# Performance work log

Hardware: AMD Instinct MI355X
Metric: run time of the kernel (lower is better)

The kernel has to match this reference:

```python
import jax, jax.numpy as jnp
from jax import lax
import numpy as np

V, T, K, R, H, EN, L = 10000, 100, 50, 300, 200, 800, 3
B = 128
TRAIN_SIZE = 100000
DELTA = 0.005


def setup_inputs():
    key = jax.random.key(0)
    ks = jax.random.split(key, 16)
    s = 0.02
    return {
        "bows": jax.random.uniform(ks[0], (B, V), jnp.float32) * 10.0 + 1e-3,
        "times": jax.random.randint(ks[1], (B,), 0, T),
        "rnn_inp": jax.random.uniform(ks[2], (T, V), jnp.float32),
        "rho_W": jax.random.normal(ks[3], (V, R), jnp.float32) * s,
        "mu_q_alpha": jax.random.normal(ks[4], (K, T, R), jnp.float32),
        "logsigma_q_alpha": jax.random.normal(ks[5], (K, T, R), jnp.float32) * 0.1 - 2.0,
        "qtheta_W1": jax.random.normal(ks[6], (EN, V + K), jnp.float32) * s,
        "qtheta_b1": jnp.zeros((EN,), jnp.float32),
        "qtheta_W2": jax.random.normal(ks[7], (EN, EN), jnp.float32) * s,
        "qtheta_b2": jnp.zeros((EN,), jnp.float32),
        "mu_theta_W": jax.random.normal(ks[8], (K, EN), jnp.float32) * s,
        "mu_theta_b": jnp.zeros((K,), jnp.float32),
        "ls_theta_W": jax.random.normal(ks[9], (K, EN), jnp.float32) * s,
        "ls_theta_b": jnp.zeros((K,), jnp.float32),
        "eta_map_W": jax.random.normal(ks[10], (H, V), jnp.float32) * s,
        "eta_map_b": jnp.zeros((H,), jnp.float32),
        "lstm_Wih": jax.random.normal(ks[11], (L, 4 * H, H), jnp.float32) * s,
        "lstm_Whh": jax.random.normal(ks[12], (L, 4 * H, H), jnp.float32) * s,
        "lstm_bih": jnp.zeros((L, 4 * H), jnp.float32),
        "lstm_bhh": jnp.zeros((L, 4 * H), jnp.float32),
        "mu_eta_W": jax.random.normal(ks[13], (K, H + K), jnp.float32) * s,
        "mu_eta_b": jnp.zeros((K,), jnp.float32),
        "ls_eta_W": jax.random.normal(ks[14], (K, H + K), jnp.float32) * s,
        "ls_eta_b": jnp.zeros((K,), jnp.float32),
    }


def _kl(q_mu, q_ls, p_mu, p_ls):
    # KL(N(q_mu, exp(q_ls)) || N(p_mu, exp(p_ls))), logsigma == log-variance as in torch code
    return 0.5 * jnp.sum((jnp.exp(q_ls) + (q_mu - p_mu) ** 2) / (jnp.exp(p_ls) + 1e-6) - 1.0 + p_ls - q_ls, axis=-1)


def _lstm(x, Wih, Whh, bih, bhh):
    # x: [T, H]; L stacked LSTM layers (batch of 1 squeezed), torch gate order i,f,g,o
    for l in range(Wih.shape[0]):
        Wi, Wh, bi, bh = Wih[l], Whh[l], bih[l], bhh[l]
        Hd = Wh.shape[1]

        def step(carry, xt, Wi=Wi, Wh=Wh, bi=bi, bh=bh):
            h, c = carry
            g = Wi @ xt + Wh @ h + bi + bh
            i, f, gg, o = jnp.split(g, 4)
            c = jax.nn.sigmoid(f) * c + jax.nn.sigmoid(i) * jnp.tanh(gg)
            h = jax.nn.sigmoid(o) * jnp.tanh(c)
            return (h, c), h

        z = jnp.zeros((Hd,), x.dtype)
        _, x = lax.scan(step, (z, z), x)
    return x


def _forward(bows, rnn_inp, rho_W, mu_q_alpha, logsigma_q_alpha, qtheta_W1, qtheta_b1, qtheta_W2, qtheta_b2, mu_theta_W, mu_theta_b, ls_theta_W, ls_theta_b, eta_map_W, eta_map_b, lstm_Wih, lstm_Whh, lstm_bih, lstm_bhh, mu_eta_W, mu_eta_b, ls_eta_W, ls_eta_b, times):
    log_delta = jnp.log(jnp.float32(DELTA))
    # --- eta: LSTM over word-freq sequence, then sequential mu/logsigma/KL per t ---
    out = _lstm(rnn_inp @ eta_map_W.T + eta_map_b, lstm_Wih, lstm_Whh, lstm_bih, lstm_bhh)  # [T,H]
    p_ls_seq = jnp.concatenate([jnp.zeros((1,), jnp.float32), jnp.full((T - 1,), log_delta, jnp.float32)])

    def eta_step(eta_prev, xs):
        o_t, p_ls = xs
        x = jnp.concatenate([o_t, eta_prev])
        mu = mu_eta_W @ x + mu_eta_b
        ls = ls_eta_W @ x + ls_eta_b
        kl = _kl(mu, ls, eta_prev, jnp.full_like(mu, p_ls))
        return mu, (mu, kl)  # eval-mode reparameterize -> eta_t = mu

    _, (etas, kls) = lax.scan(eta_step, jnp.zeros((K,), jnp.float32), (out, p_ls_seq))
    kl_eta = kls.sum()
    # --- theta encoder ---
    nb = bows / bows.sum(1, keepdims=True)
    eta_td = etas[times]  # [B,K]
    h = jax.nn.relu(jnp.concatenate([nb, eta_td], axis=1) @ qtheta_W1.T + qtheta_b1)
    h = jax.nn.relu(h @ qtheta_W2.T + qtheta_b2)
    mu_t = h @ mu_theta_W.T + mu_theta_b
    ls_t = h @ ls_theta_W.T + ls_theta_b
    theta = jax.nn.softmax(mu_t, axis=-1)  # z = mu (eval-mode reparam)
    coeff = jnp.float32(TRAIN_SIZE / bows.shape[0])
    kl_theta = _kl(mu_t, ls_t, eta_td, jnp.zeros_like(mu_t)).sum() * coeff
    # --- alpha: with eval-mode reparam, alphas == mu, so KL is fully vectorized ---
    muT = jnp.transpose(mu_q_alpha, (1, 0, 2))  # [T,K,R]
    lsT = jnp.transpose(logsigma_q_alpha, (1, 0, 2))
    alphas = muT
    p_mu = jnp.concatenate([jnp.zeros((1, K, R), muT.dtype), alphas[:-1]], axis=0)
    p_ls = jnp.concatenate([jnp.zeros((1, K, R), muT.dtype), jnp.full((T - 1, K, R), log_delta, muT.dtype)], axis=0)
    kl_alpha = _kl(muT, lsT, p_mu, p_ls).sum()
    # --- beta and NLL ---
    logit = alphas.reshape(T * K, R) @ rho_W.T  # [T*K, V]
    beta = jax.nn.softmax(logit, axis=-1).reshape(T, K, V)
    beta_d = beta[times]  # [B,K,V]
    loglik = jnp.log(jnp.einsum('bk,bkv->bv', theta, beta_d) + 1e-12)
    nll = (-(loglik * bows).sum(-1)).sum() * coeff
    loss = nll + kl_eta + kl_theta + kl_alpha
    return loss, nll, kl_eta, kl_theta, kl_alpha


def reference(bows, times, rnn_inp, rho_W, mu_q_alpha, logsigma_q_alpha, qtheta_W1, qtheta_b1, qtheta_W2, qtheta_b2, mu_theta_W, mu_theta_b, ls_theta_W, ls_theta_b, eta_map_W, eta_map_b, lstm_Wih, lstm_Whh, lstm_bih, lstm_bhh, mu_eta_W, mu_eta_b, ls_eta_W, ls_eta_b):
    return _forward(bows, rnn_inp, rho_W, mu_q_alpha, logsigma_q_alpha, qtheta_W1, qtheta_b1, qtheta_W2, qtheta_b2, mu_theta_W, mu_theta_b, ls_theta_W, ls_theta_b, eta_map_W, eta_map_b, lstm_Wih, lstm_Whh, lstm_bih, lstm_bhh, mu_eta_W, mu_eta_b, ls_eta_W, ls_eta_b, times)
```

## Files before the change

### kernel.cpp

```cpp
#include <hip/hip_runtime.h>


typedef unsigned int u32;
typedef unsigned short u16;
typedef _Float16 f16;
typedef f16 f16x2 __attribute__((ext_vector_type(2)));
typedef short bf16x8 __attribute__((ext_vector_type(8)));
typedef float f32x4 __attribute__((ext_vector_type(4)));
typedef u32 u32x4 __attribute__((ext_vector_type(4)));

#define LOG_DELTA (-5.2983174f)
#define COEFF 781.25f

#if defined(__has_builtin)
#if __has_builtin(__builtin_amdgcn_sdot4)
#define HAVE_SDOT4 1
#endif
#endif

__device__ __forceinline__ float bf2f(u16 a) { return __uint_as_float(((u32)a) << 16); }
__device__ __forceinline__ u16 f2bf(float f) {
  u32 u = __float_as_uint(f);
  u32 r = (u + 0x7fffu + ((u >> 16) & 1u)) >> 16;
  return (u16)r;
}
__device__ __forceinline__ int dot4i8(u32 a, u32 b, int c) {
#ifdef HAVE_SDOT4
  return __builtin_amdgcn_sdot4(a, b, c, false);
#else
  int s = c;
  s += ((int)(a << 24) >> 24) * ((int)(b << 24) >> 24);
  s += ((int)(a << 16) >> 24) * ((int)(b << 16) >> 24);
  s += ((int)(a << 8) >> 24) * ((int)(b << 8) >> 24);
  s += ((int)a >> 24) * ((int)b >> 24);
  return s;
#endif
}
__device__ __forceinline__ float sigm(float x) { return 1.f / (1.f + __expf(-x)); }
__device__ __forceinline__ float ftanh(float x) { float t = __expf(2.f * x); return (t - 1.f) / (t + 1.f); }
__device__ __forceinline__ u16 f2h(float x) { return __builtin_bit_cast(u16, (f16)x); }
__device__ __forceinline__ float h2f(u16 x) { return (float)__builtin_bit_cast(f16, x); }
__device__ __forceinline__ void async_load16(const u16* g, u16* l) {
  __builtin_amdgcn_global_load_lds((const __attribute__((address_space(1))) u32*)g,
                                   (__attribute__((address_space(3))) u32*)l, 16, 0, 0);
}


__global__ __launch_bounds__(64) void k_zero(float* __restrict__ accum) {
  if (threadIdx.x < 8) accum[threadIdx.x] = 0.f;
}

__global__ __launch_bounds__(256) void k_nb(const float* __restrict__ bows, float* __restrict__ nb) {
  __shared__ float red[256];
  const int b = blockIdx.x, tid = threadIdx.x;
  float s = 0.f;
  for (int v = tid; v < 10000; v += 256) s += bows[b * 10000 + v];
  red[tid] = s; __syncthreads();
  for (int o = 128; o > 0; o >>= 1) { if (tid < o) red[tid] += red[tid + o]; __syncthreads(); }
  const float inv = 1.f / red[0];
  for (int v = tid; v < 10000; v += 256) nb[b * 10000 + v] = bows[b * 10000 + v] * inv;
}

__global__ __launch_bounds__(256) void k_bsum(const float* __restrict__ a, const float* __restrict__ b,
                                              float* __restrict__ o, int n) {
  int i = blockIdx.x * 256 + threadIdx.x;
  if (i < n) o[i] = a[i] + b[i];
}

__global__ __launch_bounds__(256) void k_fill(float* __restrict__ C, const float* __restrict__ bias,
                                              int N, int total) {
  for (int i = blockIdx.x * 256 + threadIdx.x; i < total; i += gridDim.x * 256)
    C[i] = bias[i % N];
}

__global__ __launch_bounds__(256) void k_relu(float* __restrict__ C, int total) {
  for (int i = blockIdx.x * 256 + threadIdx.x; i < total; i += gridDim.x * 256) {
    float v = C[i];
    C[i] = v > 0.f ? v : 0.f;
  }
}

__global__ __launch_bounds__(128) void k_stack2(const float* __restrict__ a, const float* __restrict__ b,
                                                float* __restrict__ o) {
  const int t = threadIdx.x;
  if (t < 50) o[t] = a[t];
  else if (t < 100) o[t] = b[t - 50];
}

__global__ __launch_bounds__(64) void k_quant_whh(const float* __restrict__ Whh,
                                                  u32* __restrict__ whq, float* __restrict__ rowscale) {
  const int gr = blockIdx.x;
  const int lane = threadIdx.x;
  __shared__ float wrow[200];
  const float* src = Whh + (size_t)gr * 200;
  float m = 0.f;
  for (int c = lane; c < 200; c += 64) { float v = src[c]; wrow[c] = v; m = fmaxf(m, fabsf(v)); }
  for (int o = 32; o > 0; o >>= 1) m = fmaxf(m, __shfl_down(m, o));
  m = __shfl(m, 0);
  const float qs = (m > 0.f) ? 127.f / m : 0.f;
  __syncthreads();
  const int l = gr / 800, rr = gr - l * 800;
  if (lane < 52) {
    u32 d = 0;
    if (lane < 50) {
#pragma unroll
      for (int b = 0; b < 4; ++b) {
        int q = __float2int_rn(wrow[lane * 4 + b] * qs);
        q = max(-127, min(127, q));
        d |= ((u32)(q & 0xff)) << (8 * b);
      }
    }
    whq[l * 41600 + rr * 52 + lane] = d;
  }
  if (lane == 0) rowscale[gr] = (m > 0.f) ? m / 127.f : 0.f;
}

__global__ __launch_bounds__(256) void k_prep_A(const float* __restrict__ muq, u16* __restrict__ Abf) {
  int idx = blockIdx.x * 256 + threadIdx.x;
  if (idx >= 5120 * 320) return;
  int r = idx % 320, m = idx / 320;
  float v = 0.f;
  if (r < 300 && m < 5000) { int t = m / 50, k = m - t * 50; v = muq[k * 30000 + t * 300 + r]; }
  Abf[idx] = f2bf(v);
}
__global__ __launch_bounds__(256) void k_prep_B(const float* __restrict__ rho, u16* __restrict__ Bbf) {
  int idx = blockIdx.x * 256 + threadIdx.x;
  if (idx >= 10112 * 320) return;
  int r = idx % 320, n = idx / 320;
  float v = (r < 300 && n < 10000) ? rho[n * 300 + r] : 0.f;
  Bbf[idx] = f2bf(v);
}


#define ST 64
#define SBK 32

template<int AMODE, int BMODE, int EPI>
__global__ __launch_bounds__(256) void gemm64(
    const float* __restrict__ A, const float* __restrict__ Bm, const float* __restrict__ Bm2,
    const float* __restrict__ bias, float* __restrict__ C,
    int M, int N, int Kd, int lda, int ldb,
    const int* __restrict__ times, const float* __restrict__ etas)
{
  __shared__ __align__(16) float As[SBK][ST + 4];
  __shared__ __align__(16) float Bs[SBK][ST + 4];
  const int tid = threadIdx.x;
  const int tx = tid & 15, ty = tid >> 4;
  const int m_base = blockIdx.x * ST, n_base = blockIdx.y * ST;
  float acc[4][4] = {};
  const int nkt = (Kd + SBK - 1) / SBK;
  const int per = (nkt + gridDim.z - 1) / gridDim.z;
  const int kt0 = blockIdx.z * per;
  const int kt1 = min(nkt, kt0 + per);
  const int lkk = tid & 31;
  const int lrow = tid >> 5;
  for (int kt = kt0; kt < kt1; ++kt) {
    const int kg = kt * SBK + lkk;
#pragma unroll
    for (int i = 0; i < 8; ++i) {
      const int m = m_base + lrow + i * 8;
      float v = 0.f;
      if (m < M && kg < Kd) {
        if (AMODE == 0) v = A[(size_t)m * lda + kg];
        else {
          if (kg < 10000) v = A[(size_t)m * 10000 + kg];
          else v = etas[times[m] * 50 + (kg - 10000)];
        }
      }
      As[lkk][lrow + i * 8] = v;
    }
#pragma unroll
    for (int i = 0; i < 8; ++i) {
      const int n = n_base + lrow + i * 8;
      float v = 0.f;
      if (n < N && kg < Kd) {
        if (BMODE == 0) v = Bm[(size_t)n * ldb + kg];
        else v = (n < 50) ? Bm[(size_t)n * ldb + kg] : Bm2[(size_t)(n - 50) * ldb + kg];
      }
      Bs[lkk][lrow + i * 8] = v;
    }
    __syncthreads();
#pragma unroll
    for (int kk = 0; kk < SBK; ++kk) {
      const float4 a4 = *(const float4*)&As[kk][ty * 4];
      const float4 b4 = *(const float4*)&Bs[kk][tx * 4];
      const float av[4] = {a4.x, a4.y, a4.z, a4.w};
      const float bv[4] = {b4.x, b4.y, b4.z, b4.w};
#pragma unroll
      for (int i = 0; i < 4; ++i)
#pragma unroll
        for (int j = 0; j < 4; ++j) acc[i][j] += av[i] * bv[j];
    }
    __syncthreads();
  }
#pragma unroll
  for (int i = 0; i < 4; ++i) {
    const int m = m_base + ty * 4 + i;
    if (m >= M) continue;
#pragma unroll
    for (int j = 0; j < 4; ++j) {
      const int n = n_base + tx * 4 + j;
      if (n >= N) continue;
      float v = acc[i][j];
      if (EPI == 1) { C[(size_t)m * N + n] = v + bias[n]; }
      else if (EPI == 2) { v += bias[n]; C[(size_t)m * N + n] = v > 0.f ? v : 0.f; }
      else if (EPI == 5) { atomicAdd(&C[(size_t)m * N + n], v); }
      else { C[(size_t)m * N + n] = v; }
    }
  }
}


__global__ __launch_bounds__(256) void gemm_mfma_bT(
    const u16* __restrict__ A, const u16* __restrict__ B, u16* __restrict__ C,
    int M, int N)
{
  __shared__ u16 As[128 * 32];
  __shared__ u16 Bs[128 * 32];
  const int tid = threadIdx.x;
  const int l = tid & 63, w = tid >> 6;
  const int wm = w & 1, wn = w >> 1;
  const int m0 = blockIdx.x * 128, n0 = blockIdx.y * 128;
  f32x4 acc[4][4] = {};
  const int arow = l >> 2;
  const int acol = (l & 3) * 8;
  for (int kt = 0; kt < 10; ++kt) {
    const int k0 = kt * 32;
#pragma unroll
    for (int c = 0; c < 2; ++c) {
      const int i = w + c * 4;
      async_load16(A + (size_t)(m0 + i * 16 + arow) * 320 + k0 + acol, As + i * 512);
      async_load16(B + (size_t)(n0 + i * 16 + arow) * 320 + k0 + acol, Bs + i * 512);
    }
    __syncthreads();
    bf16x8 af[4], bfr[4];
#pragma unroll
    for (int x = 0; x < 4; ++x) {
      af[x]  = *(const bf16x8*)&As[(wm * 64 + x * 16 + (l & 15)) * 32 + (l >> 4) * 8];
      bfr[x] = *(const bf16x8*)&Bs[(wn * 64 + x * 16 + (l & 15)) * 32 + (l >> 4) * 8];
    }
#pragma unroll
    for (int x = 0; x < 4; ++x)
#pragma unroll
      for (int y = 0; y < 4; ++y)
        acc[x][y] = __builtin_amdgcn_mfma_f32_16x16x32_bf16(af[x], bfr[y], acc[x][y], 0, 0, 0);
    __syncthreads();
  }
  const int col = l & 15, quad = l >> 4;
#pragma unroll
  for (int x = 0; x < 4; ++x) {
    const int gmB = m0 + wm * 64 + x * 16 + quad * 4;
#pragma unroll
    for (int y = 0; y < 4; ++y) {
      const int gn = n0 + wn * 64 + y * 16 + col;
      if (gn >= N) continue;
#pragma unroll
      for (int r = 0; r < 4; ++r) {
        const int gm = gmB + r;
        if (gm < M) C[(size_t)gm * N + gn] = f2bf(acc[x][y][r]);
      }
    }
  }
}


__global__ __launch_bounds__(512, 1) void lstm_scan_reg(
    const u32* __restrict__ whq,
    const float* __restrict__ rowscale,
    const float* __restrict__ xproj,
    float* __restrict__ hseq)
{
  __shared__ u16 pg[800];
  __shared__ __align__(16) u32 hq[52];
  __shared__ float wmax[8];
  __shared__ float hscale_s[1];
  const int tid = threadIdx.x;
  const int act = (tid < 400);
  const int r0 = tid, r1 = tid + 400;
  u32x4 wA4[13], wB4[13];
  float rsA = 0.f, rsB = 0.f;
  float xpA = 0.f, xpB = 0.f;
  if (act) {
    const u32x4* gA = (const u32x4*)(whq + (size_t)r0 * 52);
    const u32x4* gB = (const u32x4*)(whq + (size_t)r1 * 52);
#pragma unroll
    for (int i = 0; i < 13; ++i) { wA4[i] = gA[i]; wB4[i] = gB[i]; }
    rsA = rowscale[r0]; rsB = rowscale[r1];
    xpA = xproj[r0]; xpB = xproj[r1];
  }
  if (tid < 52) hq[tid] = 0;
  if (tid < 8) wmax[tid] = 0.f;
  if (tid == 0) hscale_s[0] = 0.f;
  float c_reg = 0.f;
  __syncthreads();
  for (int t = 0; t < 100; ++t) {
    if (act) {
      float nxA = 0.f, nxB = 0.f;
      if (t < 99) { nxA = xproj[(t + 1) * 800 + r0]; nxB = xproj[(t + 1) * 800 + r1]; }
      const float hdq = hscale_s[0];
      u32x4 hv4[13];
#pragma unroll
      for (int i = 0; i < 13; ++i) hv4[i] = *((const u32x4*)hq + i);
      int aA = 0, aB = 0;
#pragma unroll
      for (int g = 0; g < 50; ++g) {
        const u32 h = hv4[g >> 2][g & 3];
        aA = dot4i8(wA4[g >> 2][g & 3], h, aA);
        aB = dot4i8(wB4[g >> 2][g & 3], h, aB);
      }
      pg[r0] = f2h((float)aA * (rsA * hdq) + xpA);
      pg[r1] = f2h((float)aB * (rsB * hdq) + xpB);
      xpA = nxA; xpB = nxB;
    }
    __syncthreads();
    float hv = 0.f;
    if (tid < 200) {
      float gi = sigm(h2f(pg[tid]));
      float gf = sigm(h2f(pg[200 + tid]));
      float gg = ftanh(h2f(pg[400 + tid]));
      float go = sigm(h2f(pg[600 + tid]));
      c_reg = gf * c_reg + gi * gg;
      hv = go * ftanh(c_reg);
      hseq[t * 200 + tid] = hv;
    }
    float m = fabsf(hv);
    for (int o = 32; o > 0; o >>= 1) m = fmaxf(m, __shfl_down(m, o));
    if ((tid & 63) == 0) wmax[tid >> 6] = m;
    __syncthreads();
    if (tid < 200) {
      const float hm = fmaxf(fmaxf(wmax[0], wmax[1]), fmaxf(wmax[2], wmax[3]));
      const float qs = (hm > 0.f) ? 127.f / hm : 0.f;
      int q = __float2int_rn(hv * qs);
      q = max(-127, min(127, q));
      ((signed char*)hq)[tid] = (signed char)q;
      if (tid == 0) hscale_s[0] = (hm > 0.f) ? hm / 127.f : 0.f;
    }
    __syncthreads();
  }
}


__global__ __launch_bounds__(64, 1) void eta_scan_reg(
    const float* __restrict__ muW, const float* __restrict__ lsW,
    const float* __restrict__ pc0,
    float* __restrict__ etas, float* __restrict__ accum)
{
  __shared__ __align__(16) float ep[52];
  const int j = threadIdx.x;
  const int act = (j < 50);
  float wmu[52], wls[52];
  if (act) {
#pragma unroll
    for (int k = 0; k < 25; ++k) {
      float2 a = *(const float2*)(muW + (size_t)j * 250 + 200 + 2 * k);
      float2 b = *(const float2*)(lsW + (size_t)j * 250 + 200 + 2 * k);
      wmu[2 * k] = a.x; wmu[2 * k + 1] = a.y;
      wls[2 * k] = b.x; wls[2 * k + 1] = b.y;
    }
    wmu[50] = wmu[51] = wls[50] = wls[51] = 0.f;
  } else {
#pragma unroll
    for (int k = 0; k < 52; ++k) { wmu[k] = 0.f; wls[k] = 0.f; }
  }
  if (j < 52) ep[j] = 0.f;
  float klacc = 0.f;
  float mye = 0.f;
  float pmu = act ? pc0[j] : 0.f;
  float pls_ = act ? pc0[50 + j] : 0.f;
  __syncthreads();
  for (int t = 0; t < 100; ++t) {
    float nmu = 0.f, nls = 0.f;
    if (act && t < 99) { nmu = pc0[(t + 1) * 100 + j]; nls = pc0[(t + 1) * 100 + 50 + j]; }
    float ma[4] = {pmu, 0.f, 0.f, 0.f};
    float la[4] = {pls_, 0.f, 0.f, 0.f};
    const float4* e4 = (const float4*)ep;
#pragma unroll
    for (int i = 0; i < 13; ++i) {
      const float4 e = e4[i];
      ma[0] += wmu[4 * i + 0] * e.x; ma[1] += wmu[4 * i + 1] * e.y;
      ma[2] += wmu[4 * i + 2] * e.z; ma[3] += wmu[4 * i + 3] * e.w;
      la[0] += wls[4 * i + 0] * e.x; la[1] += wls[4 * i + 1] * e.y;
      la[2] += wls[4 * i + 2] * e.z; la[3] += wls[4 * i + 3] * e.w;
    }
    const float mu = (ma[0] + ma[1]) + (ma[2] + ma[3]);
    const float ls = (la[0] + la[1]) + (la[2] + la[3]);
    __syncthreads();
    if (act) {
      const float pls = (t == 0) ? 0.f : LOG_DELTA;
      const float pv = __expf(pls) + 1e-6f;
      const float d = mu - mye;
      klacc += 0.5f * ((__expf(ls) + d * d) / pv - 1.f + pls - ls);
      etas[t * 50 + j] = mu;
      mye = mu;
      ep[j] = mu;
    }
    __syncthreads();
    pmu = nmu; pls_ = nls;
  }
  for (int o = 32; o > 0; o >>= 1) klacc += __shfl_down(klacc, o);
  if (j == 0) accum[0] = klacc;
}


__global__ __launch_bounds__(64) void k_theta(const float* __restrict__ mul,
                                              const float* __restrict__ etas, const int* __restrict__ times,
                                              float* __restrict__ theta, float* __restrict__ accum) {
  const int b = blockIdx.x, lane = threadIdx.x;
  float m_ = 0.f, l_ = 0.f, e_ = 0.f, mx = -1e30f;
  if (lane < 50) {
    m_ = mul[b * 100 + lane];
    l_ = mul[b * 100 + 50 + lane];
    e_ = etas[times[b] * 50 + lane];
    mx = m_;
  }
  for (int o = 32; o > 0; o >>= 1) mx = fmaxf(mx, __shfl_down(mx, o));
  mx = __shfl(mx, 0);
  float ex = (lane < 50) ? __expf(m_ - mx) : 0.f;
  float sum = ex;
  for (int o = 32; o > 0; o >>= 1) sum += __shfl_down(sum, o);
  sum = __shfl(sum, 0);
  if (lane < 50) theta[b * 50 + lane] = ex / sum;
  float kl = 0.f;
  if (lane < 50) {
    float d = m_ - e_;
    kl = 0.5f * ((__expf(l_) + d * d) / (1.f + 1e-6f) - 1.f - l_);
  }
  for (int o = 32; o > 0; o >>= 1) kl += __shfl_down(kl, o);
  if (lane == 0) atomicAdd(accum + 1, kl);
}


__global__ __launch_bounds__(256) void k_rowsum(const u16* __restrict__ logit, float* __restrict__ Z) {
  const int r = blockIdx.x, tid = threadIdx.x;
  const u32* row = (const u32*)(logit + (size_t)r * 10000);
  __shared__ float red[256];
  float s = 0.f;
  for (int v = tid; v < 5000; v += 256) {
    u32 p = row[v];
    s += __expf(bf2f((u16)(p & 0xffffu))) + __expf(bf2f((u16)(p >> 16)));
  }
  red[tid] = s; __syncthreads();
  for (int o = 128; o > 0; o >>= 1) { if (tid < o) red[tid] += red[tid + o]; __syncthreads(); }
  if (tid == 0) Z[r] = red[0];
}


__global__ __launch_bounds__(256) void k_nll(const u16* __restrict__ logit, const float* __restrict__ Z,
                                             const float* __restrict__ theta, const float* __restrict__ bows,
                                             const int* __restrict__ times, float* __restrict__ accum) {
  const int b = blockIdx.x, seg = blockIdx.y, tid = threadIdx.x;
  const int t = times[b];
  __shared__ float c2[52];
  __shared__ float red[256];
  if (tid < 50) c2[tid] = theta[b * 50 + tid] / Z[t * 50 + tid];
  __syncthreads();
  float part = 0.f;
  const int v0 = seg * 1250, v1 = v0 + 1250;
  const u16* base = logit + (size_t)t * 500000;
  for (int v = v0 + tid; v < v1; v += 256) {
    float ssv = 1e-12f;
#pragma unroll
    for (int k = 0; k < 50; ++k) ssv += c2[k] * __expf(bf2f(base[k * 10000 + v]));
    part += bows[b * 10000 + v] * __logf(ssv);
  }
  red[tid] = part; __syncthreads();
  for (int o = 128; o > 0; o >>= 1) { if (tid < o) red[tid] += red[tid + o]; __syncthreads(); }
  if (tid == 0) atomicAdd(accum + 3, -red[0]);
}


__global__ __launch_bounds__(256) void k_alpha_kl(const float* __restrict__ muq, const float* __restrict__ lsq,
                                                  float* __restrict__ accum) {
  __shared__ float red[256];
  const int tid = threadIdx.x;
  float s = 0.f;
  for (int i = blockIdx.x * 256 + tid; i < 1500000; i += gridDim.x * 256) {
    int r = i % 300;
    int tk = i / 300;
    int k = tk % 50;
    int t = tk / 50;
    size_t idx = (size_t)k * 30000 + (size_t)t * 300 + r;
    float mu = muq[idx], ls = lsq[idx];
    float pm = 0.f, pls = 0.f;
    if (t > 0) { pm = muq[idx - 300]; pls = LOG_DELTA; }
    float d = mu - pm;
    s += 0.5f * ((__expf(ls) + d * d) / (__expf(pls) + 1e-6f) - 1.f + pls - ls);
  }
  red[tid] = s; __syncthreads();
  for (int o = 128; o > 0; o >>= 1) { if (tid < o) red[tid] += red[tid + o]; __syncthreads(); }
  if (tid == 0) atomicAdd(accum + 2, red[0]);
}


__global__ __launch_bounds__(64) void k_final(const float* __restrict__ accum, float* __restrict__ out) {
  if (threadIdx.x == 0) {
    float nll = accum[3] * COEFF;
    float kl_eta = accum[0];
    float kl_theta = accum[1] * COEFF;
    float kl_alpha = accum[2];
    out[0] = nll + kl_eta + kl_theta + kl_alpha;
    out[1] = nll;
    out[2] = kl_eta;
    out[3] = kl_theta;
    out[4] = kl_alpha;
  }
}


extern "C" void kernel_launch(void* const* d_in, const int* in_sizes, int n_in,
                              void* d_out, int out_size, void* d_ws, size_t ws_size,
                              hipStream_t stream) {
  (void)in_sizes; (void)n_in; (void)out_size; (void)ws_size;
  const float* bows   = (const float*)d_in[0];
  const int*   times  = (const int*)d_in[1];
  const float* rnn_in = (const float*)d_in[2];
  const float* rho_W  = (const float*)d_in[3];
  const float* muq    = (const float*)d_in[4];
  const float* lsq    = (const float*)d_in[5];
  const float* qW1    = (const float*)d_in[6];
  const float* qb1    = (const float*)d_in[7];
  const float* qW2    = (const float*)d_in[8];
  const float* qb2    = (const float*)d_in[9];
  const float* muthW  = (const float*)d_in[10];
  const float* muthb  = (const float*)d_in[11];
  const float* lsthW  = (const float*)d_in[12];
  const float* lsthb  = (const float*)d_in[13];
  const float* emW    = (const float*)d_in[14];
  const float* emb    = (const float*)d_in[15];
  const float* Wih    = (const float*)d_in[16];
  const float* Whh    = (const float*)d_in[17];
  const float* bih    = (const float*)d_in[18];
  const float* bhh    = (const float*)d_in[19];
  const float* mueW   = (const float*)d_in[20];
  const float* mueb   = (const float*)d_in[21];
  const float* lseW   = (const float*)d_in[22];
  const float* lseb   = (const float*)d_in[23];
  float* out = (float*)d_out;
  float* ws = (float*)d_ws;

  float* accum = ws + 0;
  float* nb    = ws + 8;
  float* x0    = ws + 1280008;
  float* xproj = ws + 1300008;
  float* hsA   = ws + 1380008;
  float* hsB   = ws + 1400008;
  u32*   whq   = (u32*)(ws + 1420008);
  float* rowsc = ws + 1544808;
  float* bias2 = ws + 1547208;
  float* pc0   = ws + 1547408;
  float* bias2e= ws + 1558008;
  float* hsC   = ws + 1560008;
  float* bsum  = ws + 1660008;
  float* etas  = ws + 1662408;
  float* h1    = ws + 1667408;
  float* h2    = ws + 1769808;
  float* mul   = ws + 1872208;
  float* theta = ws + 1885008;
  float* Zrow  = ws + 1891408;
  u16*   A_bf  = (u16*)(ws + 1896408);
  u16*   B_bf  = (u16*)(ws + 2715608);
  u16*   logit = (u16*)(ws + 4333528);

  k_zero<<<1, 64, 0, stream>>>(accum);
  k_nb<<<128, 256, 0, stream>>>(bows, nb);
  k_quant_whh<<<2400, 64, 0, stream>>>(Whh, whq, rowsc);
  k_bsum<<<10, 256, 0, stream>>>(bih, bhh, bsum, 2400);
  k_prep_A<<<6400, 256, 0, stream>>>(muq, A_bf);
  k_prep_B<<<12640, 256, 0, stream>>>(rho_W, B_bf);
  k_stack2<<<1, 128, 0, stream>>>(muthb, lsthb, bias2);
  k_stack2<<<1, 128, 0, stream>>>(mueb, lseb, bias2e);
  k_fill<<<40, 256, 0, stream>>>(pc0, bias2e, 100, 10000);

  k_fill<<<79, 256, 0, stream>>>(x0, emb, 200, 20000);
  gemm64<0, 0, 5><<<dim3(2, 4, 32), 256, 0, stream>>>(rnn_in, emW, nullptr, nullptr, x0,
                                                      100, 200, 10000, 10000, 10000, nullptr, nullptr);

  const float* lin[3] = {x0, hsA, hsB};
  float* lout[3] = {hsA, hsB, hsC};
  for (int l = 0; l < 3; ++l) {
    gemm64<0, 0, 1><<<dim3(2, 13, 1), 256, 0, stream>>>(lin[l], Wih + l * 160000, nullptr,
                                                        bsum + l * 800, xproj,
                                                        100, 800, 200, 200, 200, nullptr, nullptr);
    lstm_scan_reg<<<1, 512, 0, stream>>>(whq + l * 41600, rowsc + l * 800, xproj, lout[l]);
  }
  gemm64<0, 1, 5><<<dim3(2, 2, 7), 256, 0, stream>>>(hsC, mueW, lseW, nullptr, pc0,
                                                     100, 100, 200, 200, 250, nullptr, nullptr);
  eta_scan_reg<<<1, 64, 0, stream>>>(mueW, lseW, pc0, etas, accum);

  k_fill<<<400, 256, 0, stream>>>(h1, qb1, 800, 102400);
  gemm64<2, 0, 5><<<dim3(2, 13, 24), 256, 0, stream>>>(nb, qW1, nullptr, nullptr, h1,
                                                       128, 800, 10050, 10000, 10050, times, etas);
  k_relu<<<400, 256, 0, stream>>>(h1, 102400);
  k_fill<<<400, 256, 0, stream>>>(h2, qb2, 800, 102400);
  gemm64<0, 0, 5><<<dim3(2, 13, 4), 256, 0, stream>>>(h1, qW2, nullptr, nullptr, h2,
                                                      128, 800, 800, 800, 800, nullptr, nullptr);
  k_relu<<<400, 256, 0, stream>>>(h2, 102400);
  k_fill<<<50, 256, 0, stream>>>(mul, bias2, 100, 12800);
  gemm64<0, 1, 5><<<dim3(2, 2, 5), 256, 0, stream>>>(h2, muthW, lsthW, nullptr, mul,
                                                     128, 100, 800, 800, 800, nullptr, nullptr);
  k_theta<<<128, 64, 0, stream>>>(mul, etas, times, theta, accum);

  gemm_mfma_bT<<<dim3(40, 79), 256, 0, stream>>>(A_bf, B_bf, logit, 5000, 10000);
  k_rowsum<<<5000, 256, 0, stream>>>(logit, Zrow);
  k_nll<<<dim3(128, 8), 256, 0, stream>>>(logit, Zrow, theta, bows, times, accum);

  k_alpha_kl<<<512, 256, 0, stream>>>(muq, lsq, accum);
  k_final<<<1, 64, 0, stream>>>(accum, out);
}
```

Baseline: 1.153 ms.

## Add 128x128 register-prefetched split-K SGEMM for large-K embedding and encoder GEMMs

Introduces a new FP32 GEMM kernel with 128x128 tiles, 8x8 per-thread micro-tiles, padded shared memory and register prefetch of the next K-tile, using split-K with atomic accumulation. It replaces the 64-tile GEMM for the rnn embedding projection (K=10000) and the first q_theta layer (K=10050). The larger tiles raise arithmetic intensity and reduce redundant global loads for these wide-K products. In exchange the kernel uses more registers and has fewer M/N blocks, and the number of atomic adds changes with the new split-K factor.

```diff
diff --git a/kernel.cpp b/kernel.cpp
--- a/kernel.cpp
+++ b/kernel.cpp
@@ -206,6 +206,100 @@
       else if (EPI == 2) { v += bias[n]; C[(size_t)m * N + n] = v > 0.f ? v : 0.f; }
       else if (EPI == 5) { atomicAdd(&C[(size_t)m * N + n], v); }
       else { C[(size_t)m * N + n] = v; }
+    }
+  }
+}
+
+
+#define LT 128
+#define LBK 32
+
+template<int AMODE>
+__global__ __launch_bounds__(256) void gemm128(
+    const float* __restrict__ A, const float* __restrict__ Bm,
+    float* __restrict__ C,
+    int M, int N, int Kd, int lda, int ldb,
+    const int* __restrict__ times, const float* __restrict__ etas)
+{
+  __shared__ __align__(16) float As[LBK][LT + 4];
+  __shared__ __align__(16) float Bs[LBK][LT + 4];
+  const int tid = threadIdx.x;
+  const int tx = tid & 15, ty = tid >> 4;
+  const int m_base = blockIdx.x * LT, n_base = blockIdx.y * LT;
+  const int nkt = (Kd + LBK - 1) / LBK;
+  const int per = (nkt + gridDim.z - 1) / gridDim.z;
+  const int kt0 = blockIdx.z * per;
+  const int kt1 = min(nkt, kt0 + per);
+  if (kt0 >= kt1) return;
+  const int lkk = tid & 31;
+  const int lrow = tid >> 5;
+  float acc[8][8] = {};
+  float pa[16], pb[16];
+  {
+    const int kg = kt0 * LBK + lkk;
+#pragma unroll
+    for (int i = 0; i < 16; ++i) {
+      const int m = m_base + lrow + i * 8;
+      float v = 0.f;
+      if (m < M && kg < Kd) {
+        if (AMODE == 0) v = A[(size_t)m * lda + kg];
+        else v = (kg < 10000) ? A[(size_t)m * 10000 + kg] : etas[times[m] * 50 + (kg - 10000)];
+      }
+      pa[i] = v;
+      const int n = n_base + lrow + i * 8;
+      float w = 0.f;
+      if (n < N && kg < Kd) w = Bm[(size_t)n * ldb + kg];
+      pb[i] = w;
+    }
+  }
+  for (int kt = kt0; kt < kt1; ++kt) {
+#pragma unroll
+    for (int i = 0; i < 16; ++i) {
+      As[lkk][lrow + i * 8] = pa[i];
+      Bs[lkk][lrow + i * 8] = pb[i];
+    }
+    __syncthreads();
+    if (kt + 1 < kt1) {
+      const int kg = (kt + 1) * LBK + lkk;
+#pragma unroll
+      for (int i = 0; i < 16; ++i) {
+        const int m = m_base + lrow + i * 8;
+        float v = 0.f;
+        if (m < M && kg < Kd) {
+          if (AMODE == 0) v = A[(size_t)m * lda + kg];
+          else v = (kg < 10000) ? A[(size_t)m * 10000 + kg] : etas[times[m] * 50 + (kg - 10000)];
+        }
+        pa[i] = v;
+        const int n = n_base + lrow + i * 8;
+        float w = 0.f;
+        if (n < N && kg < Kd) w = Bm[(size_t)n * ldb + kg];
+        pb[i] = w;
+      }
+    }
+#pragma unroll
+    for (int kk = 0; kk < LBK; ++kk) {
+      const float4* ap = (const float4*)&As[kk][ty * 8];
+      const float4* bp = (const float4*)&Bs[kk][tx * 8];
+      const float4 a0 = ap[0], a1 = ap[1];
+      const float4 b0 = bp[0], b1 = bp[1];
+      const float av[8] = {a0.x, a0.y, a0.z, a0.w, a1.x, a1.y, a1.z, a1.w};
+      const float bv[8] = {b0.x, b0.y, b0.z, b0.w, b1.x, b1.y, b1.z, b1.w};
+#pragma unroll
+      for (int i = 0; i < 8; ++i)
+#pragma unroll
+        for (int j = 0; j < 8; ++j) acc[i][j] += av[i] * bv[j];
+    }
+    __syncthreads();
+  }
+#pragma unroll
+  for (int i = 0; i < 8; ++i) {
+    const int m = m_base + ty * 8 + i;
+    if (m >= M) continue;
+#pragma unroll
+    for (int j = 0; j < 8; ++j) {
+      const int n = n_base + tx * 8 + j;
+      if (n >= N) continue;
+      atomicAdd(&C[(size_t)m * N + n], acc[i][j]);
     }
   }
 }
@@ -572,8 +666,8 @@
   k_fill<<<40, 256, 0, stream>>>(pc0, bias2e, 100, 10000);
 
   k_fill<<<79, 256, 0, stream>>>(x0, emb, 200, 20000);
-  gemm64<0, 0, 5><<<dim3(2, 4, 32), 256, 0, stream>>>(rnn_in, emW, nullptr, nullptr, x0,
-                                                      100, 200, 10000, 10000, 10000, nullptr, nullptr);
+  gemm128<0><<<dim3(1, 2, 104), 256, 0, stream>>>(rnn_in, emW, x0,
+                                                  100, 200, 10000, 10000, 10000, nullptr, nullptr);
 
   const float* lin[3] = {x0, hsA, hsB};
   float* lout[3] = {hsA, hsB, hsC};
@@ -588,8 +682,8 @@
   eta_scan_reg<<<1, 64, 0, stream>>>(mueW, lseW, pc0, etas, accum);
 
   k_fill<<<400, 256, 0, stream>>>(h1, qb1, 800, 102400);
-  gemm64<2, 0, 5><<<dim3(2, 13, 24), 256, 0, stream>>>(nb, qW1, nullptr, nullptr, h1,
-                                                       128, 800, 10050, 10000, 10050, times, etas);
+  gemm128<2><<<dim3(1, 7, 45), 256, 0, stream>>>(nb, qW1, h1,
+                                                 128, 800, 10050, 10000, 10050, times, etas);
   k_relu<<<400, 256, 0, stream>>>(h1, 102400);
   k_fill<<<400, 256, 0, stream>>>(h2, qb2, 800, 102400);
   gemm64<0, 0, 5><<<dim3(2, 13, 4), 256, 0, stream>>>(h1, qW2, nullptr, nullptr, h2,
```

New measurement: 1.337 ms. +15.9%, slower.
